# Performance work log

Measured on AMD Instinct MI355X. Metric: run time of the kernel, lower is better.

## Reference

```python
import jax, jax.numpy as jnp
import numpy as np

B, S, H = 2, 1024, 768
D, HID = 24, 96            # hdim_proj_dim, hdim_mlp_hidden
VIN, VHID = 3 * H, 2 * max(128, H // 2)  # concat_hadam -> 3H; out_hid = 768
ALPHA0 = 0.05              # init_gate_hdim


def setup_inputs() -> dict:
    key = jax.random.key(0)
    ks = jax.random.split(key, 10)
    sc = 0.02
    return {
        "H_j": jax.random.normal(ks[0], (B, S, H), jnp.float32),
        "H_i": jax.random.normal(ks[1], (B, S, H), jnp.float32),
        "attn_mask": jnp.ones((B, S), jnp.float32),
        "Wpj": jax.random.normal(ks[2], (H, D), jnp.float32) * sc,
        "Wpi": jax.random.normal(ks[3], (H, D), jnp.float32) * sc,
        "W1": jax.random.normal(ks[4], (4 * D, HID), jnp.float32) * sc,
        "b1": jnp.zeros((HID,), jnp.float32),
        "W2": jax.random.normal(ks[5], (HID, 1), jnp.float32) * sc,
        "b2": jnp.zeros((1,), jnp.float32),
        "Wv1": jax.random.normal(ks[6], (VIN, VHID), jnp.float32) * sc,
        "bv1": jnp.zeros((VHID,), jnp.float32),
        "Wv2": jax.random.normal(ks[7], (VHID, H), jnp.float32) * sc,
        "bv2": jnp.zeros((H,), jnp.float32),
        "alpha": jnp.float32(ALPHA0),
    }


def reference(H_j, H_i, attn_mask, Wpj, Wpi, W1, b1, W2, b2, Wv1, bv1, Wv2, bv2, alpha):
    # token projections: [B,S,D]
    Zj = H_j @ Wpj
    Zi = H_i @ Wpi
    # 4-term pair MLP, decomposed so the [B,S,S,4D] concat is never built:
    # cat([Zj_pair, Zi_pair, Zj*Zi, |Zj-Zi|]) @ W1 == sum of 4 partial products
    W1a, W1b, W1c, W1d = W1[:D], W1[D:2 * D], W1[2 * D:3 * D], W1[3 * D:]
    tj = Zj @ W1a                                   # [B,S,HID]
    ti = Zi @ W1b                                   # [B,S,HID]
    had = jnp.einsum('bsd,btd,dh->bsth', Zj, Zi, W1c)          # [B,S,S,HID]
    diff = jnp.abs(Zj[:, :, None, :] - Zi[:, None, :, :]) @ W1d  # [B,S,S,HID]
    h = jax.nn.relu(tj[:, :, None, :] + ti[:, None, :, :] + had + diff + b1)
    logits = (h @ W2)[..., 0] + b2[0]               # [B,S,S]
    # additive mask on key axis (torch: (1-mask)*finfo.min)
    logits = logits + (1.0 - attn_mask[:, None, :]) * jnp.finfo(logits.dtype).min
    probs = jax.nn.softmax(logits, axis=-1)
    ctx = jnp.einsum('bst,bth->bsh', probs, H_i)    # context over H_i
    # value fusion: concat_hadam -> [ctx, H_j, ctx*H_j]
    msg_in = jnp.concatenate([ctx, H_j, ctx * H_j], axis=-1)
    msg = jax.nn.relu(msg_in @ Wv1 + bv1) @ Wv2 + bv2
    return alpha * msg  # dropout is identity at eval
```

## Files before the change

kernel.cpp:

```cpp
#include <hip/hip_runtime.h>
#include <math.h>

#define BB   2
#define SS   1024
#define HH   768
#define DD   24
#define HIDD 96
#define VINN 2304
#define VHIDD 768
#define NRR  2048

typedef __attribute__((ext_vector_type(8))) short short8;
typedef __attribute__((ext_vector_type(4))) float floatx4;

static __device__ inline unsigned short f2bf(float x) {
    unsigned int u = __float_as_uint(x);
    u = (u + 0x7FFFu + ((u >> 16) & 1u)) >> 16;
    return (unsigned short)u;
}
static __device__ inline unsigned int pack2(float a, float b) {
    return (unsigned int)f2bf(a) | ((unsigned int)f2bf(b) << 16);
}

static __device__ inline void gl16(const unsigned short* g, unsigned short* l) {
    __builtin_amdgcn_global_load_lds(
        (const __attribute__((address_space(1))) unsigned int*)g,
        (__attribute__((address_space(3))) unsigned int*)l,
        16, 0, 0);
}

__global__ __launch_bounds__(256) void k_tconv(
    const float* __restrict__ in, unsigned short* __restrict__ out,
    int R, int C)
{
    size_t zoff = (size_t)blockIdx.z * R * C;
    in += zoff; out += zoff;
    __shared__ float tile[32][33];
    int r0 = blockIdx.y * 32, c0 = blockIdx.x * 32;
    int tc = threadIdx.x & 31, tr = threadIdx.x >> 5;
    #pragma unroll
    for (int i = 0; i < 4; ++i)
        tile[tr + i*8][tc] = in[(size_t)(r0 + tr + i*8)*C + c0 + tc];
    __syncthreads();
    #pragma unroll
    for (int i = 0; i < 4; ++i)
        out[(size_t)(c0 + tr + i*8)*R + r0 + tc] = f2bf(tile[tc][tr + i*8]);
}

__global__ __launch_bounds__(256) void k_zproj(
    const float* __restrict__ Hj, const float* __restrict__ Hi,
    const float* __restrict__ Wpj, const float* __restrict__ Wpi,
    unsigned* __restrict__ Zjp, unsigned* __restrict__ Zip)
{
    __shared__ __align__(16) unsigned short sA[64][72];
    __shared__ __align__(16) unsigned short sBT[32][72];
    int tid = threadIdx.x;
    int w = tid >> 6, lane = tid & 63;
    int quad = lane >> 4, col = lane & 15;

    int m0 = blockIdx.x * 64;
    bool isJ = (m0 < NRR);
    const float* src = isJ ? Hj : Hi;
    const float* Wp  = isJ ? Wpj : Wpi;
    unsigned* Zp     = isJ ? Zjp : Zip;
    int rowbase = isJ ? m0 : (m0 - NRR);

    floatx4 acc[2];
    acc[0] = (floatx4){0.f,0.f,0.f,0.f};
    acc[1] = (floatx4){0.f,0.f,0.f,0.f};

    for (int kb = 0; kb < HH; kb += 64) {
        #pragma unroll
        for (int i = 0; i < 4; ++i) {
            int f4 = tid + i*256;
            int r = f4 >> 4, c4 = f4 & 15;
            float4 v = *(const float4*)(src + (size_t)(rowbase + r)*HH + kb + c4*4);
            uint2 pkt; pkt.x = pack2(v.x, v.y); pkt.y = pack2(v.z, v.w);
            *(uint2*)&sA[r][c4*4] = pkt;
        }
        {
            const float* wsrc = Wp + (size_t)kb*DD;
            #pragma unroll
            for (int i = 0; i < 6; ++i) {
                int idx = tid + i*256;
                int k = idx / DD, n = idx % DD;
                sBT[n][k] = f2bf(wsrc[idx]);
            }
        }
        __syncthreads();
        #pragma unroll
        for (int kt = 0; kt < 2; ++kt) {
            short8 av = *(const short8*)&sA[w*16 + col][kt*32 + quad*8];
            #pragma unroll
            for (int nt = 0; nt < 2; ++nt) {
                short8 bv = *(const short8*)&sBT[nt*16 + col][kt*32 + quad*8];
                acc[nt] = __builtin_amdgcn_mfma_f32_16x16x32_bf16(av, bv, acc[nt], 0, 0, 0);
            }
        }
        __syncthreads();
    }
    #pragma unroll
    for (int nt = 0; nt < 2; ++nt) {
        #pragma unroll
        for (int r = 0; r < 4; ++r) {
            float v = acc[nt][r];
            float vn = __shfl_xor(v, 1, 64);
            int n = nt*16 + col;
            if (!(col & 1) && n < DD) {
                int m = w*16 + quad*4 + r;
                Zp[(size_t)(rowbase + m)*12 + (n >> 1)] = pack2(v, vn);
            }
        }
    }
}

#define LSTR 72
#define TC 128
__global__ __launch_bounds__(256) void k_attn(
    const unsigned* __restrict__ Zjp, const unsigned* __restrict__ Zip,
    const float* __restrict__ W1, const float* __restrict__ b1,
    const float* __restrict__ W2,
    const float* __restrict__ mask, unsigned short* __restrict__ probs)
{
    int row = blockIdx.x;
    int b = row >> 10;
    int tid = threadIdx.x;
    int lane = tid & 63, wv = tid >> 6;
    int quad = lane >> 4, col = lane & 15;

    __shared__ __align__(16) unsigned short sAB[2][TC*LSTR];
    __shared__ __align__(16) float sLog[SS];
    __shared__ unsigned sZjp[12];
    __shared__ float sW2[HIDD];
    __shared__ float sRed[4];

    if (tid < 12) sZjp[tid] = Zjp[(size_t)row*12 + tid];
    if (tid < HIDD) sW2[tid] = W2[tid];
    __syncthreads();

    if (tid < HIDD) {
        int h = tid;
        float zj[24];
        #pragma unroll
        for (int u = 0; u < 12; ++u) {
            unsigned z = sZjp[u];
            zj[2*u]   = __uint_as_float(z << 16);
            zj[2*u+1] = __uint_as_float(z & 0xffff0000u);
        }
        float tj = b1[h];
        #pragma unroll
        for (int d = 0; d < DD; ++d) tj = fmaf(zj[d], W1[d*HIDD + h], tj);
        unsigned short* rowp = &sAB[0][h*LSTR];
        #pragma unroll
        for (int d = 0; d < DD; ++d)
            rowp[d] = f2bf(fmaf(zj[d], W1[(48+d)*HIDD + h], W1[(24+d)*HIDD + h]));
        #pragma unroll
        for (int d = 0; d < DD; ++d)
            rowp[24+d] = f2bf(W1[(72+d)*HIDD + h]);
        rowp[48] = f2bf(tj);
        #pragma unroll
        for (int k = 49; k < 64; ++k) rowp[k] = 0;
    }
    __syncthreads();

    short8 bfr[6][2];
    #pragma unroll
    for (int nf = 0; nf < 6; ++nf)
        #pragma unroll
        for (int kt = 0; kt < 2; ++kt)
            bfr[nf][kt] = *(const short8*)&sAB[0][(nf*16 + col)*LSTR + kt*32 + quad*8];
    float4 w2q[6];
    #pragma unroll
    for (int nf = 0; nf < 6; ++nf)
        w2q[nf] = *(const float4*)&sW2[nf*16 + quad*4];
    __syncthreads();

    {
        int r = tid >> 1, bf = tid & 1;
        unsigned short* rowp = &sAB[bf][r*LSTR];
        uint4 w0; w0.x = 0x3F80u; w0.y = 0; w0.z = 0; w0.w = 0;
        *(uint4*)&rowp[48] = w0;
        uint4 zz; zz.x = 0; zz.y = 0; zz.z = 0; zz.w = 0;
        *(uint4*)&rowp[56] = zz;
    }

    int t_loc = tid >> 1, hh = tid & 1;
    const unsigned* zbase = Zip + (size_t)(b << 10) * 12;

    auto pack = [&](int chunk, int bf) {
        int t = chunk*TC + t_loc;
        const unsigned* zr = zbase + (size_t)t*12;
        unsigned short* rowp = &sAB[bf][t_loc*LSTR];
        uint4 first = *(const uint4*)(zr + hh*4);
        *(uint4*)&rowp[hh*8] = first;
        uint2 ext; ext.x = 0; ext.y = 0;
        if (hh) {
            uint4 second = *(const uint4*)(zr + 8);
            *(uint4*)&rowp[16] = second;
            unsigned myz[6] = {first.z, first.w, second.x, second.y, second.z, second.w};
            unsigned q[6];
            #pragma unroll
            for (int u = 0; u < 6; ++u) {
                unsigned za = sZjp[6 + u], zb = myz[u];
                float alo = __uint_as_float(za << 16);
                float ahi = __uint_as_float(za & 0xffff0000u);
                float blo = __uint_as_float(zb << 16);
                float bhi = __uint_as_float(zb & 0xffff0000u);
                unsigned dlo = __float_as_uint(fabsf(alo - blo)) + 0x8000u;
                unsigned dhi = __float_as_uint(fabsf(ahi - bhi)) + 0x8000u;
                q[u] = __builtin_amdgcn_perm(dhi, dlo, 0x07060302u);
            }
            #pragma unroll
            for (int j = 0; j < 3; ++j) {
                uint2 wq; wq.x = q[2*j]; wq.y = q[2*j+1];
                *(uint2*)&rowp[36 + 4*j] = wq;
            }
        } else {
            ext = *(const uint2*)(zr + 4);
            unsigned myz[6] = {first.x, first.y, first.z, first.w, ext.x, ext.y};
            unsigned q[6];
            #pragma unroll
            for (int u = 0; u < 6; ++u) {
                unsigned za = sZjp[u], zb = myz[u];
                float alo = __uint_as_float(za << 16);
                float ahi = __uint_as_float(za & 0xffff0000u);
                float blo = __uint_as_float(zb << 16);
                float bhi = __uint_as_float(zb & 0xffff0000u);
                unsigned dlo = __float_as_uint(fabsf(alo - blo)) + 0x8000u;
                unsigned dhi = __float_as_uint(fabsf(ahi - bhi)) + 0x8000u;
                q[u] = __builtin_amdgcn_perm(dhi, dlo, 0x07060302u);
            }
            #pragma unroll
            for (int j = 0; j < 3; ++j) {
                uint2 wq; wq.x = q[2*j]; wq.y = q[2*j+1];
                *(uint2*)&rowp[24 + 4*j] = wq;
            }
        }
    };

    pack(0, 0);
    __syncthreads();

    for (int chunk = 0; chunk < SS/TC; ++chunk) {
        int cur = chunk & 1;
        if (chunk + 1 < SS/TC) pack(chunk + 1, cur ^ 1);

        short8 av[2][2];
        #pragma unroll
        for (int tt = 0; tt < 2; ++tt) {
            int arow = (wv*2 + tt)*16 + col;
            av[tt][0] = *(const short8*)&sAB[cur][arow*LSTR + quad*8];
            av[tt][1] = *(const short8*)&sAB[cur][arow*LSTR + 32 + quad*8];
        }
        float s0 = 0.f, s1 = 0.f;
        #pragma unroll
        for (int hf = 0; hf < 6; ++hf) {
            floatx4 a0 = {0.f,0.f,0.f,0.f}, a1 = {0.f,0.f,0.f,0.f};
            a0 = __builtin_amdgcn_mfma_f32_16x16x32_bf16(bfr[hf][0], av[0][0], a0, 0, 0, 0);
            a0 = __builtin_amdgcn_mfma_f32_16x16x32_bf16(bfr[hf][1], av[0][1], a0, 0, 0, 0);
            a1 = __builtin_amdgcn_mfma_f32_16x16x32_bf16(bfr[hf][0], av[1][0], a1, 0, 0, 0);
            a1 = __builtin_amdgcn_mfma_f32_16x16x32_bf16(bfr[hf][1], av[1][1], a1, 0, 0, 0);
            float w2v[4] = {w2q[hf].x, w2q[hf].y, w2q[hf].z, w2q[hf].w};
            #pragma unroll
            for (int r = 0; r < 4; ++r) {
                s0 = fmaf(fmaxf(a0[r], 0.f), w2v[r], s0);
                s1 = fmaf(fmaxf(a1[r], 0.f), w2v[r], s1);
            }
        }
        s0 += __shfl_xor(s0, 16, 64);  s0 += __shfl_xor(s0, 32, 64);
        s1 += __shfl_xor(s1, 16, 64);  s1 += __shfl_xor(s1, 32, 64);
        if (lane < 16) {
            sLog[chunk*TC + (wv*2 + 0)*16 + lane] = s0;
            sLog[chunk*TC + (wv*2 + 1)*16 + lane] = s1;
        }
        __syncthreads();
    }

    float lv[4];
    #pragma unroll
    for (int i = 0; i < 4; ++i) {
        int t = tid + i*256;
        lv[i] = sLog[t] + (1.0f - mask[(size_t)(b<<10) + t]) * (-3.402823466e+38f);
    }
    float m = fmaxf(fmaxf(lv[0], lv[1]), fmaxf(lv[2], lv[3]));
    #pragma unroll
    for (int off = 32; off; off >>= 1) m = fmaxf(m, __shfl_down(m, off, 64));
    if (lane == 0) sRed[wv] = m;
    __syncthreads();
    float M = fmaxf(fmaxf(sRed[0], sRed[1]), fmaxf(sRed[2], sRed[3]));
    float e[4]; float ssum = 0.f;
    #pragma unroll
    for (int i = 0; i < 4; ++i) { e[i] = expf(lv[i] - M); ssum += e[i]; }
    #pragma unroll
    for (int off = 32; off; off >>= 1) ssum += __shfl_down(ssum, off, 64);
    __syncthreads();
    if (lane == 0) sRed[wv] = ssum;
    __syncthreads();
    float inv = 1.0f / (sRed[0] + sRed[1] + sRed[2] + sRed[3]);
    #pragma unroll
    for (int i = 0; i < 4; ++i)
        probs[(size_t)row*SS + tid + i*256] = f2bf(e[i] * inv);
}

__global__ __launch_bounds__(256) void k_mgemm_p(
    const unsigned short* __restrict__ A,
    const unsigned short* __restrict__ BT,
    float* __restrict__ P,
    int K, int bt_bstride)
{
    __shared__ __align__(16) unsigned short sA[128*64];
    __shared__ __align__(16) unsigned short sB[128*64];
    int tid = threadIdx.x;
    int w = tid >> 6, lane = tid & 63;
    int quad = lane >> 4, col = lane & 15;

    int n0 = blockIdx.x * 128, m0 = blockIdx.y * 128;
    int z = blockIdx.z;
    int kslice = K >> 2;
    int k0 = z * kslice;
    int nk = kslice >> 6;
    const unsigned short* Bb = BT + (size_t)(m0 >> 10) * bt_bstride;

    int srow = lane >> 3;
    int skc  = (lane & 7) * 8;

    floatx4 acc[2][8];
    #pragma unroll
    for (int mt = 0; mt < 2; ++mt)
        #pragma unroll
        for (int nf = 0; nf < 8; ++nf)
            acc[mt][nf] = (floatx4){0.f,0.f,0.f,0.f};

    for (int kb = 0; kb < nk; ++kb) {
        int kofs = k0 + kb*64;
        #pragma unroll
        for (int i = 0; i < 4; ++i) {
            int rbase = w*8 + i*32;
            gl16(A  + (size_t)(m0 + rbase + srow)*K + kofs + skc, &sA[rbase*64]);
            gl16(Bb + (size_t)(n0 + rbase + srow)*K + kofs + skc, &sB[rbase*64]);
        }
        __syncthreads();
        #pragma unroll
        for (int kt = 0; kt < 2; ++kt) {
            short8 av[2];
            #pragma unroll
            for (int mt = 0; mt < 2; ++mt)
                av[mt] = *(const short8*)&sA[(w*32 + mt*16 + col)*64 + kt*32 + quad*8];
            #pragma unroll
            for (int nf = 0; nf < 8; ++nf) {
                short8 bv = *(const short8*)&sB[(nf*16 + col)*64 + kt*32 + quad*8];
                #pragma unroll
                for (int mt = 0; mt < 2; ++mt)
                    acc[mt][nf] = __builtin_amdgcn_mfma_f32_16x16x32_bf16(
                        av[mt], bv, acc[mt][nf], 0, 0, 0);
            }
        }
        __syncthreads();
    }

    float* Pz = P + (size_t)z*NRR*768;
    #pragma unroll
    for (int mt = 0; mt < 2; ++mt) {
        #pragma unroll
        for (int nf = 0; nf < 8; ++nf) {
            int n = n0 + nf*16 + col;
            #pragma unroll
            for (int r = 0; r < 4; ++r) {
                int m = w*32 + mt*16 + quad*4 + r;
                Pz[(size_t)(m0 + m)*768 + n] = acc[mt][nf][r];
            }
        }
    }
}

template<int MODE>
__global__ __launch_bounds__(256) void k_epi(
    const float* __restrict__ P,
    const float* __restrict__ bias,
    const float* __restrict__ Hj,
    const float* __restrict__ alpha_p,
    void* __restrict__ Cout)
{
    int idx = blockIdx.x*256 + threadIdx.x;
    int g = idx / 192, c = (idx % 192) * 4;
    float v[4] = {0.f, 0.f, 0.f, 0.f};
    #pragma unroll
    for (int z = 0; z < 4; ++z) {
        float4 vz = *(const float4*)(P + (size_t)z*NRR*768 + (size_t)g*768 + c);
        v[0] += vz.x; v[1] += vz.y; v[2] += vz.z; v[3] += vz.w;
    }
    if (MODE == 0) {
        float4 h4 = *(const float4*)(Hj + (size_t)g*HH + c);
        float hj[4] = {h4.x, h4.y, h4.z, h4.w};
        unsigned short* msgin = (unsigned short*)Cout;
        uint2 wc, wh, wp;
        wc.x = pack2(v[0], v[1]);        wc.y = pack2(v[2], v[3]);
        wh.x = pack2(hj[0], hj[1]);      wh.y = pack2(hj[2], hj[3]);
        wp.x = pack2(v[0]*hj[0], v[1]*hj[1]);
        wp.y = pack2(v[2]*hj[2], v[3]*hj[3]);
        *(uint2*)&msgin[(size_t)g*VINN + c]        = wc;
        *(uint2*)&msgin[(size_t)g*VINN + HH + c]   = wh;
        *(uint2*)&msgin[(size_t)g*VINN + 2*HH + c] = wp;
    } else if (MODE == 1) {
        float4 b4 = *(const float4*)(bias + c);
        uint2 wy;
        wy.x = pack2(fmaxf(v[0]+b4.x, 0.f), fmaxf(v[1]+b4.y, 0.f));
        wy.y = pack2(fmaxf(v[2]+b4.z, 0.f), fmaxf(v[3]+b4.w, 0.f));
        *(uint2*)&((unsigned short*)Cout)[(size_t)g*VHIDD + c] = wy;
    } else {
        float a = alpha_p[0];
        float4 b4 = *(const float4*)(bias + c);
        float4 o;
        o.x = a*(v[0]+b4.x); o.y = a*(v[1]+b4.y);
        o.z = a*(v[2]+b4.z); o.w = a*(v[3]+b4.w);
        *(float4*)&((float*)Cout)[(size_t)g*HH + c] = o;
    }
}

extern "C" void kernel_launch(void* const* d_in, const int* in_sizes, int n_in,
                              void* d_out, int out_size, void* d_ws, size_t ws_size,
                              hipStream_t stream)
{
    const float* Hj   = (const float*)d_in[0];
    const float* Hi   = (const float*)d_in[1];
    const float* mask = (const float*)d_in[2];
    const float* Wpj  = (const float*)d_in[3];
    const float* Wpi  = (const float*)d_in[4];
    const float* W1   = (const float*)d_in[5];
    const float* b1   = (const float*)d_in[6];
    const float* W2   = (const float*)d_in[7];
    const float* Wv1  = (const float*)d_in[9];
    const float* bv1  = (const float*)d_in[10];
    const float* Wv2  = (const float*)d_in[11];
    const float* bv2  = (const float*)d_in[12];
    const float* alpha = (const float*)d_in[13];
    float* out = (float*)d_out;

    const int NR = NRR;
    char* p = (char*)d_ws;
    auto alloc = [&](size_t bytes) {
        char* r = p; p += (bytes + 255) & ~(size_t)255; return r;
    };
    unsigned* Zjp          = (unsigned*)alloc((size_t)NR*12*4);
    unsigned* Zip          = (unsigned*)alloc((size_t)NR*12*4);
    unsigned short* probsb = (unsigned short*)alloc((size_t)NR*SS*2);
    unsigned short* HiT    = (unsigned short*)alloc((size_t)BB*HH*SS*2);
    unsigned short* Wv1T   = (unsigned short*)alloc((size_t)VHIDD*VINN*2);
    unsigned short* Wv2T   = (unsigned short*)alloc((size_t)HH*VHIDD*2);
    unsigned short* msginb = (unsigned short*)alloc((size_t)NR*VINN*2);
    unsigned short* Y1b    = (unsigned short*)alloc((size_t)NR*VHIDD*2);
    float* Part            = (float*)alloc((size_t)4*NR*768*4);

    k_tconv<<<dim3(VHIDD/32, VINN/32, 1), 256, 0, stream>>>(Wv1, Wv1T, VINN, VHIDD);
    k_tconv<<<dim3(HH/32, VHIDD/32, 1), 256, 0, stream>>>(Wv2, Wv2T, VHIDD, HH);
    k_tconv<<<dim3(HH/32, SS/32, BB), 256, 0, stream>>>(Hi, HiT, SS, HH);
    k_zproj<<<2*NR/64, 256, 0, stream>>>(Hj, Hi, Wpj, Wpi, Zjp, Zip);
    k_attn<<<NR, 256, 0, stream>>>(Zjp, Zip, W1, b1, W2, mask, probsb);

    const int EPI_GRID = NR*192/256;

    k_mgemm_p<<<dim3(HH/128, NR/128, 4), 256, 0, stream>>>(
        probsb, HiT, Part, SS, HH*SS);
    k_epi<0><<<EPI_GRID, 256, 0, stream>>>(Part, nullptr, Hj, alpha, msginb);

    k_mgemm_p<<<dim3(VHIDD/128, NR/128, 4), 256, 0, stream>>>(
        msginb, Wv1T, Part, VINN, 0);
    k_epi<1><<<EPI_GRID, 256, 0, stream>>>(Part, bv1, nullptr, alpha, Y1b);

    k_mgemm_p<<<dim3(HH/128, NR/128, 4), 256, 0, stream>>>(
        Y1b, Wv2T, Part, VHIDD, 0);
    k_epi<2><<<EPI_GRID, 256, 0, stream>>>(Part, bv2, nullptr, alpha, out);
}
```

Baseline: 227.5 us.

## Fuse split-K reduction and epilogue into GEMM via last-block atomic ticket

Each split-K GEMM now writes its partial tile to a per-tile scratch slot, and the last of the four K-slice blocks to arrive (found with an atomic counter) reduces the partials and applies the epilogue. This removes the three separate epilogue kernel launches and their full-size partial-buffer passes. The N tile shrinks from 128 to 64, doubling the block count to improve occupancy. In exchange it adds threadfence and atomic traffic, a memset of the counters, and lower per-block MFMA reuse from the narrower tile.

After: 574.0 us. +152.3%, slower.

```diff
diff --git a/kernel.cpp b/kernel.cpp
--- a/kernel.cpp
+++ b/kernel.cpp
@@ -302,19 +302,26 @@
         probs[(size_t)row*SS + tid + i*256] = f2bf(e[i] * inv);
 }
 
-__global__ __launch_bounds__(256) void k_mgemm_p(
+template<int MODE>
+__global__ __launch_bounds__(256) void k_mgemm_f(
     const unsigned short* __restrict__ A,
     const unsigned short* __restrict__ BT,
-    float* __restrict__ P,
+    float* __restrict__ P, int* __restrict__ ctr,
+    const float* __restrict__ bias,
+    const float* __restrict__ Hj,
+    const float* __restrict__ alpha_p,
+    void* __restrict__ Cout,
     int K, int bt_bstride)
 {
     __shared__ __align__(16) unsigned short sA[128*64];
-    __shared__ __align__(16) unsigned short sB[128*64];
+    __shared__ __align__(16) unsigned short sB[64*64];
+    __shared__ int sTicket;
     int tid = threadIdx.x;
     int w = tid >> 6, lane = tid & 63;
     int quad = lane >> 4, col = lane & 15;
 
-    int n0 = blockIdx.x * 128, m0 = blockIdx.y * 128;
+    int n0 = blockIdx.x * 64, m0 = blockIdx.y * 128;
+    int tile = blockIdx.y * gridDim.x + blockIdx.x;
     int z = blockIdx.z;
     int kslice = K >> 2;
     int k0 = z * kslice;
@@ -324,19 +331,23 @@
     int srow = lane >> 3;
     int skc  = (lane & 7) * 8;
 
-    floatx4 acc[2][8];
+    floatx4 acc[2][4];
     #pragma unroll
     for (int mt = 0; mt < 2; ++mt)
         #pragma unroll
-        for (int nf = 0; nf < 8; ++nf)
+        for (int nf = 0; nf < 4; ++nf)
             acc[mt][nf] = (floatx4){0.f,0.f,0.f,0.f};
 
     for (int kb = 0; kb < nk; ++kb) {
         int kofs = k0 + kb*64;
         #pragma unroll
         for (int i = 0; i < 4; ++i) {
-            int rbase = w*8 + i*32;
-            gl16(A  + (size_t)(m0 + rbase + srow)*K + kofs + skc, &sA[rbase*64]);
+            int rbase = w*32 + i*8;
+            gl16(A + (size_t)(m0 + rbase + srow)*K + kofs + skc, &sA[rbase*64]);
+        }
+        #pragma unroll
+        for (int i = 0; i < 2; ++i) {
+            int rbase = w*16 + i*8;
             gl16(Bb + (size_t)(n0 + rbase + srow)*K + kofs + skc, &sB[rbase*64]);
         }
         __syncthreads();
@@ -347,7 +358,7 @@
             for (int mt = 0; mt < 2; ++mt)
                 av[mt] = *(const short8*)&sA[(w*32 + mt*16 + col)*64 + kt*32 + quad*8];
             #pragma unroll
-            for (int nf = 0; nf < 8; ++nf) {
+            for (int nf = 0; nf < 4; ++nf) {
                 short8 bv = *(const short8*)&sB[(nf*16 + col)*64 + kt*32 + quad*8];
                 #pragma unroll
                 for (int mt = 0; mt < 2; ++mt)
@@ -358,62 +369,65 @@
         __syncthreads();
     }
 
-    float* Pz = P + (size_t)z*NRR*768;
+    float* Pz = P + ((size_t)tile*4 + z)*(128*64);
     #pragma unroll
     for (int mt = 0; mt < 2; ++mt) {
         #pragma unroll
-        for (int nf = 0; nf < 8; ++nf) {
-            int n = n0 + nf*16 + col;
+        for (int nf = 0; nf < 4; ++nf) {
+            int n = nf*16 + col;
             #pragma unroll
             for (int r = 0; r < 4; ++r) {
                 int m = w*32 + mt*16 + quad*4 + r;
-                Pz[(size_t)(m0 + m)*768 + n] = acc[mt][nf][r];
-            }
-        }
-    }
-}
-
-template<int MODE>
-__global__ __launch_bounds__(256) void k_epi(
-    const float* __restrict__ P,
-    const float* __restrict__ bias,
-    const float* __restrict__ Hj,
-    const float* __restrict__ alpha_p,
-    void* __restrict__ Cout)
-{
-    int idx = blockIdx.x*256 + threadIdx.x;
-    int g = idx / 192, c = (idx % 192) * 4;
-    float v[4] = {0.f, 0.f, 0.f, 0.f};
-    #pragma unroll
-    for (int z = 0; z < 4; ++z) {
-        float4 vz = *(const float4*)(P + (size_t)z*NRR*768 + (size_t)g*768 + c);
-        v[0] += vz.x; v[1] += vz.y; v[2] += vz.z; v[3] += vz.w;
-    }
-    if (MODE == 0) {
-        float4 h4 = *(const float4*)(Hj + (size_t)g*HH + c);
-        float hj[4] = {h4.x, h4.y, h4.z, h4.w};
-        unsigned short* msgin = (unsigned short*)Cout;
-        uint2 wc, wh, wp;
-        wc.x = pack2(v[0], v[1]);        wc.y = pack2(v[2], v[3]);
-        wh.x = pack2(hj[0], hj[1]);      wh.y = pack2(hj[2], hj[3]);
-        wp.x = pack2(v[0]*hj[0], v[1]*hj[1]);
-        wp.y = pack2(v[2]*hj[2], v[3]*hj[3]);
-        *(uint2*)&msgin[(size_t)g*VINN + c]        = wc;
-        *(uint2*)&msgin[(size_t)g*VINN + HH + c]   = wh;
-        *(uint2*)&msgin[(size_t)g*VINN + 2*HH + c] = wp;
-    } else if (MODE == 1) {
-        float4 b4 = *(const float4*)(bias + c);
-        uint2 wy;
-        wy.x = pack2(fmaxf(v[0]+b4.x, 0.f), fmaxf(v[1]+b4.y, 0.f));
-        wy.y = pack2(fmaxf(v[2]+b4.z, 0.f), fmaxf(v[3]+b4.w, 0.f));
-        *(uint2*)&((unsigned short*)Cout)[(size_t)g*VHIDD + c] = wy;
-    } else {
-        float a = alpha_p[0];
-        float4 b4 = *(const float4*)(bias + c);
-        float4 o;
-        o.x = a*(v[0]+b4.x); o.y = a*(v[1]+b4.y);
-        o.z = a*(v[2]+b4.z); o.w = a*(v[3]+b4.w);
-        *(float4*)&((float*)Cout)[(size_t)g*HH + c] = o;
+                Pz[m*64 + n] = acc[mt][nf][r];
+            }
+        }
+    }
+
+    __threadfence();
+    __syncthreads();
+    if (tid == 0) sTicket = atomicAdd(&ctr[tile], 1);
+    __syncthreads();
+    if (sTicket != 3) return;
+
+    __threadfence();
+    const float* Pt = P + (size_t)tile*4*(128*64);
+    float alpha = (MODE == 2) ? alpha_p[0] : 1.0f;
+    #pragma unroll
+    for (int i = 0; i < 8; ++i) {
+        int e = i*256 + tid;
+        int m = e >> 4, c4 = (e & 15)*4;
+        float4 v = *(const float4*)(Pt + m*64 + c4);
+        #pragma unroll
+        for (int zz = 1; zz < 4; ++zz) {
+            float4 vz = *(const float4*)(Pt + zz*(128*64) + m*64 + c4);
+            v.x += vz.x; v.y += vz.y; v.z += vz.z; v.w += vz.w;
+        }
+        size_t g = (size_t)(m0 + m);
+        int n = n0 + c4;
+        if (MODE == 0) {
+            float4 h4 = *(const float4*)(Hj + g*HH + n);
+            unsigned short* msgin = (unsigned short*)Cout;
+            uint2 wc, wh, wp;
+            wc.x = pack2(v.x, v.y);          wc.y = pack2(v.z, v.w);
+            wh.x = pack2(h4.x, h4.y);        wh.y = pack2(h4.z, h4.w);
+            wp.x = pack2(v.x*h4.x, v.y*h4.y);
+            wp.y = pack2(v.z*h4.z, v.w*h4.w);
+            *(uint2*)&msgin[g*VINN + n]        = wc;
+            *(uint2*)&msgin[g*VINN + HH + n]   = wh;
+            *(uint2*)&msgin[g*VINN + 2*HH + n] = wp;
+        } else if (MODE == 1) {
+            float4 b4 = *(const float4*)(bias + n);
+            uint2 wy;
+            wy.x = pack2(fmaxf(v.x+b4.x, 0.f), fmaxf(v.y+b4.y, 0.f));
+            wy.y = pack2(fmaxf(v.z+b4.z, 0.f), fmaxf(v.w+b4.w, 0.f));
+            *(uint2*)&((unsigned short*)Cout)[g*VHIDD + n] = wy;
+        } else {
+            float4 b4 = *(const float4*)(bias + n);
+            float4 o;
+            o.x = alpha*(v.x+b4.x); o.y = alpha*(v.y+b4.y);
+            o.z = alpha*(v.z+b4.z); o.w = alpha*(v.w+b4.w);
+            *(float4*)&((float*)Cout)[g*HH + n] = o;
+        }
     }
 }
 
@@ -449,7 +463,10 @@
     unsigned short* Wv2T   = (unsigned short*)alloc((size_t)HH*VHIDD*2);
     unsigned short* msginb = (unsigned short*)alloc((size_t)NR*VINN*2);
     unsigned short* Y1b    = (unsigned short*)alloc((size_t)NR*VHIDD*2);
-    float* Part            = (float*)alloc((size_t)4*NR*768*4);
+    float* Part            = (float*)alloc((size_t)192*4*128*64*4);
+    int*   Ctr             = (int*)alloc((size_t)3*192*4);
+
+    hipMemsetAsync(Ctr, 0, (size_t)3*192*4, stream);
 
     k_tconv<<<dim3(VHIDD/32, VINN/32, 1), 256, 0, stream>>>(Wv1, Wv1T, VINN, VHIDD);
     k_tconv<<<dim3(HH/32, VHIDD/32, 1), 256, 0, stream>>>(Wv2, Wv2T, VHIDD, HH);
@@ -457,17 +474,12 @@
     k_zproj<<<2*NR/64, 256, 0, stream>>>(Hj, Hi, Wpj, Wpi, Zjp, Zip);
     k_attn<<<NR, 256, 0, stream>>>(Zjp, Zip, W1, b1, W2, mask, probsb);
 
-    const int EPI_GRID = NR*192/256;
-
-    k_mgemm_p<<<dim3(HH/128, NR/128, 4), 256, 0, stream>>>(
-        probsb, HiT, Part, SS, HH*SS);
-    k_epi<0><<<EPI_GRID, 256, 0, stream>>>(Part, nullptr, Hj, alpha, msginb);
-
-    k_mgemm_p<<<dim3(VHIDD/128, NR/128, 4), 256, 0, stream>>>(
-        msginb, Wv1T, Part, VINN, 0);
-    k_epi<1><<<EPI_GRID, 256, 0, stream>>>(Part, bv1, nullptr, alpha, Y1b);
-
-    k_mgemm_p<<<dim3(HH/128, NR/128, 4), 256, 0, stream>>>(
-        Y1b, Wv2T, Part, VHIDD, 0);
-    k_epi<2><<<EPI_GRID, 256, 0, stream>>>(Part, bv2, nullptr, alpha, out);
-}
+    k_mgemm_f<0><<<dim3(HH/64, NR/128, 4), 256, 0, stream>>>(
+        probsb, HiT, Part, Ctr + 0*192, nullptr, Hj, alpha, msginb, SS, HH*SS);
+
+    k_mgemm_f<1><<<dim3(VHIDD/64, NR/128, 4), 256, 0, stream>>>(
+        msginb, Wv1T, Part, Ctr + 1*192, bv1, nullptr, alpha, Y1b, VINN, 0);
+
+    k_mgemm_f<2><<<dim3(HH/64, NR/128, 4), 256, 0, stream>>>(
+        Y1b, Wv2T, Part, Ctr + 2*192, bv2, nullptr, alpha, out, VHIDD, 0);
+}
```
